# Performance work log

Hardware: AMD Instinct MI355X
Metric: run time of the kernel (lower is better)

## Reference

```python
import math
import jax, jax.numpy as jnp
import numpy as np

STRATEGY = 'small'
K_PEAKS = 2
BW = math.radians(15.0)
HIGH_RATIO = 0.3
LOW_RATIO = 0.2
ALPHA = 1.2
BETA = 0.8
N_BINS = 180


def setup_inputs() -> dict:
    key = jax.random.key(0)
    k1, k2, k3 = jax.random.split(key, 3)
    x = jax.random.normal(k1, (16, 256, 128, 128), dtype=jnp.float32)
    w_in = jax.random.normal(k2, (16, 256), dtype=jnp.float32) * 0.06    # proj_in 1x1 conv weight [c_mid, C]
    w_out = jax.random.normal(k3, (256, 16), dtype=jnp.float32) * 0.25   # proj_out 1x1 conv weight [C, c_mid]
    return {"x": x, "w_in": w_in, "w_out": w_out}


def _forward(x, w_in, w_out):
    B, C, H, W = x.shape
    pi = jnp.float32(math.pi)
    cy, cx = H // 2, W // 2
    y = jnp.arange(H, dtype=jnp.float32)[:, None]
    xg = jnp.arange(W, dtype=jnp.float32)[None, :]
    r = jnp.sqrt((y - cy) ** 2 + (xg - cx) ** 2)                 # [H, W]
    theta = jnp.arctan2(y - cy, xg - cx) + pi                    # [H, W] in [0, 2pi]
    r_max = float(min(cy, cx))

    # 1x1 conv in
    x_proj = jnp.einsum('mc,bchw->bmhw', w_in, x)                # [B, c_mid, H, W]

    fs = jnp.fft.fftshift(jnp.fft.fft2(x_proj, norm='ortho'), axes=(-2, -1))
    mag = jnp.abs(fs)                                            # [B, c_mid, H, W]

    # ---- peak direction detection (180-bin angular histogram of high-freq energy) ----
    theta_mod = theta % pi
    high_mask = (r > HIGH_RATIO * r_max).astype(jnp.float32)     # [H, W]
    bin_edges = jnp.linspace(0.0, math.pi, N_BINS + 1, dtype=jnp.float32)
    mag_avg = mag.mean(axis=1)                                   # [B, H, W]
    weighted = (mag_avg * high_mask).reshape(B, -1)              # [B, H*W]
    bin_idx = jnp.clip(jnp.searchsorted(bin_edges, theta_mod.reshape(-1), side='left') - 1, 0, N_BINS - 1)
    energy = jax.vmap(lambda w: jax.ops.segment_sum(w, bin_idx, num_segments=N_BINS))(weighted)  # [B, 180]

    # smooth with [0.25, 0.5, 0.25], zero padding
    ep = jnp.pad(energy, ((0, 0), (1, 1)))
    es = 0.25 * ep[:, :-2] + 0.5 * ep[:, 1:-1] + 0.25 * ep[:, 2:]  # [B, 180]

    mean_e = es.mean(axis=-1, keepdims=True)
    is_peak = (es > mean_e) & (es > jnp.roll(es, 1, axis=-1)) & (es > jnp.roll(es, -1, axis=-1))
    vals = jnp.where(is_peak, es, -jnp.inf)
    topv, topi = jax.lax.top_k(vals, K_PEAKS)                    # [B, k]
    count = jnp.sum(topv > -jnp.inf, axis=-1)                    # [B] number of valid peaks (<= k)
    amax = jnp.argmax(es, axis=-1)                               # fallback when no peak found
    topi = jnp.where((count > 0)[:, None], topi, amax[:, None])
    eff = jnp.maximum(count, 1)
    pos = jnp.minimum(jnp.arange(K_PEAKS)[None, :], (eff - 1)[:, None])  # pad with last valid peak
    final_idx = jnp.take_along_axis(topi, pos, axis=1)           # [B, k]
    bin_center = (bin_edges[:-1] + bin_edges[1:]) * 0.5
    peak_angles = bin_center[final_idx]                          # [B, k]

    # ---- gain map (channel-independent) ----
    if STRATEGY == 'small':
        pa = peak_angles
        base_mask = high_mask
    else:
        pa = (peak_angles + pi / 2) % pi
        base_mask = (r <= LOW_RATIO * r_max).astype(jnp.float32)
    diff = jnp.abs(theta[None, None] - pa[:, :, None, None])     # [B, k, H, W]
    diff = jnp.minimum(diff, pi - diff)
    in_region = (diff <= BW) & (base_mask[None, None] > 0)
    enh = jnp.any(in_region, axis=1).astype(jnp.float32)         # [B, H, W]
    gain = jnp.where(enh > 0, jnp.float32(ALPHA), jnp.float32(1.0))
    other_high = high_mask[None] * (1.0 - enh)
    gain = gain * (1.0 - other_high) + other_high * BETA         # [B, H, W]

    fs_enh = fs * gain[:, None, :, :]
    x_enh = jnp.fft.ifft2(jnp.fft.ifftshift(fs_enh, axes=(-2, -1)), norm='ortho').real
    out = jnp.einsum('cm,bmhw->bchw', w_out, x_enh)
    return x + out


def reference(x, w_in, w_out):
    return _forward(x, w_in, w_out)
```

## Files before the change

kernel.cpp:

```cpp
#include <hip/hip_runtime.h>
#include <math.h>

#define NPX 16384

static constexpr float  PI_F   = 3.14159265358979323846f;
static constexpr double PI_D   = 3.14159265358979323846;
static constexpr double STEP_D = PI_D / 180.0;
static constexpr double BW_D   = 15.0 * (PI_D / 180.0);

typedef float f4 __attribute__((ext_vector_type(4)));
typedef float f2 __attribute__((ext_vector_type(2)));

__device__ __forceinline__ int swz(int r, int c) {
    return (r << 7) | (c ^ (r ^ (r >> 1)));
}
__device__ __forceinline__ int brev7(int x) { return (int)(__brev((unsigned)x) >> 25); }
__device__ __forceinline__ float2 cadd(float2 a, float2 b){ return make_float2(a.x+b.x, a.y+b.y); }
__device__ __forceinline__ float2 csub(float2 a, float2 b){ return make_float2(a.x-b.x, a.y-b.y); }
__device__ __forceinline__ float2 cmul(float2 a, float re, float im){
    return make_float2(a.x*re - a.y*im, a.x*im + a.y*re);
}
__device__ __forceinline__ double edge_d(int i) {
    return (i >= 180) ? PI_D : (double)i * STEP_D;
}

__global__ void k0_tables(double* __restrict__ theta_d, int* __restrict__ bin_hi,
                          double* __restrict__ energy) {
    int p = blockIdx.x * blockDim.x + threadIdx.x;
    if (p < NPX) {
        int h = p >> 7, w = p & 127;
        double dy = (double)(h - 64), dx = (double)(w - 64);
        double theta = atan2(dy, dx) + PI_D;
        theta_d[p] = theta;
        double v = fmod(theta, PI_D);
        int cnt = 0;
        for (int i = 0; i <= 180; ++i) cnt += (edge_d(i) < v) ? 1 : 0;
        int bin = cnt - 1;
        if (bin < 0) bin = 0;
        if (bin > 179) bin = 179;
        int r2 = (h - 64)*(h - 64) + (w - 64)*(w - 64);
        bool high = (r2 >= 369);
        bin_hi[p] = high ? bin : -1;
    }
    if (blockIdx.x == 0) {
        for (int i = threadIdx.x; i < 16 * 180; i += blockDim.x) energy[i] = 0.0;
    }
}

__global__ __launch_bounds__(256, 1) void k1_proj(const float* __restrict__ x,
        const float* __restrict__ w_in, float* __restrict__ xproj) {
    int b  = blockIdx.y;
    int t4 = blockIdx.x * blockDim.x + threadIdx.x;
    const f4* xb = (const f4*)(x + (size_t)b * 256 * NPX);
    f4 acc[16];
    #pragma unroll
    for (int m = 0; m < 16; ++m) acc[m] = (f4)0.0f;
    #pragma unroll 8
    for (int c = 0; c < 256; ++c) {
        f4 xv = xb[(size_t)c * (NPX/4) + t4];
        #pragma unroll
        for (int m = 0; m < 16; ++m) {
            float wv = w_in[m * 256 + c];
            acc[m] += wv * xv;
        }
    }
    f4* xp = (f4*)(xproj + (size_t)b * 16 * NPX);
    #pragma unroll
    for (int m = 0; m < 16; ++m) xp[(size_t)m * (NPX/4) + t4] = acc[m];
}

__global__ __launch_bounds__(1024) void k_fft_fwd(const float* __restrict__ xproj,
        float2* __restrict__ fs, const int* __restrict__ bin_hi,
        double* __restrict__ energy) {
    extern __shared__ float2 lds[];
    __shared__ float twr[64], twi[64];
    __shared__ double histp[8][180];
    const int tid = threadIdx.x;
    const int img = blockIdx.x;
    if (tid < 64) {
        float ang = (float)tid * (PI_F / 64.0f);
        twr[tid] = cosf(ang);
        twi[tid] = sinf(ang);
    }
    if (tid < 180) {
        #pragma unroll
        for (int g = 0; g < 8; ++g) histp[g][tid] = 0.0;
    }
    const float* src = xproj + (size_t)img * NPX;
    #pragma unroll
    for (int it = 0; it < 16; ++it) {
        int p = tid + it * 1024;
        lds[swz(p >> 7, p & 127)] = make_float2(src[p], 0.0f);
    }
    __syncthreads();
    #pragma unroll
    for (int dim = 0; dim < 2; ++dim) {
        #pragma unroll
        for (int s = 0; s <= 4; s += 2) {
            const int q = 32 >> s;
            #pragma unroll
            for (int it = 0; it < 4; ++it) {
                int fb = tid + it * 1024;
                int o = fb & 127;
                int bfi = fb >> 7;
                int p = bfi & (q - 1);
                int g = bfi >> (5 - s);
                int P = g * (128 >> s) + p;
                int k1 = p << s;
                float tc = twr[k1],   ts = twi[k1];
                float uc = twr[2*k1], us = twi[2*k1];
                int e0, e1, e2, e3;
                if (dim == 0) { e0=swz(o,P); e1=swz(o,P+q); e2=swz(o,P+2*q); e3=swz(o,P+3*q); }
                else          { e0=swz(P,o); e1=swz(P+q,o); e2=swz(P+2*q,o); e3=swz(P+3*q,o); }
                float2 a = lds[e0], b = lds[e1], c = lds[e2], d = lds[e3];
                float2 u0 = cadd(a, c);
                float2 u1 = cmul(csub(a, c), tc, -ts);
                float2 v0 = cadd(b, d);
                float2 v1 = cmul(csub(b, d), -ts, -tc);
                lds[e0] = cadd(u0, v0);
                lds[e1] = cmul(csub(u0, v0), uc, -us);
                lds[e2] = cadd(u1, v1);
                lds[e3] = cmul(csub(u1, v1), uc, -us);
            }
            __syncthreads();
        }
        #pragma unroll
        for (int it = 0; it < 8; ++it) {
            int fb = tid + it * 1024;
            int o = fb & 127;
            int g = fb >> 7;
            int e0, e1;
            if (dim == 0) { e0 = swz(o, 2*g); e1 = swz(o, 2*g+1); }
            else          { e0 = swz(2*g, o); e1 = swz(2*g+1, o); }
            float2 a = lds[e0], b = lds[e1];
            lds[e0] = cadd(a, b);
            lds[e1] = csub(a, b);
        }
        __syncthreads();
    }
    float2* dst = fs + (size_t)img * NPX;
    const int bofs = (img >> 4) * 180;
    const int grp = tid >> 7;
    #pragma unroll
    for (int it = 0; it < 16; ++it) {
        int p = tid + it * 1024;
        int r = p >> 7, c = p & 127;
        float2 v = lds[swz(r, c)];
        dst[p] = v;
        int pix = ((brev7(r) ^ 64) << 7) | (brev7(c) ^ 64);
        int bh = bin_hi[pix];
        if (bh >= 0) {
            double m = sqrt((double)v.x * (double)v.x + (double)v.y * (double)v.y);
            atomicAdd(&histp[grp][bh], m);
        }
    }
    __syncthreads();
    if (tid < 180) {
        double s = 0.0;
        #pragma unroll
        for (int g = 0; g < 8; ++g) s += histp[g][tid];
        atomicAdd(&energy[bofs + tid], s);
    }
}

__global__ void k3_peaks(const double* __restrict__ energy, const double* __restrict__ theta_d,
                         const int* __restrict__ bin_hi, float* __restrict__ gain_s) {
    __shared__ double e[180], es[180];
    __shared__ double pa[2];
    int b = blockIdx.x, tid = threadIdx.x;
    if (tid < 180) e[tid] = energy[b * 180 + tid];
    __syncthreads();
    if (tid < 180) {
        double l = (tid > 0)   ? e[tid-1] : 0.0;
        double r = (tid < 179) ? e[tid+1] : 0.0;
        es[tid] = 0.25*l + 0.5*e[tid] + 0.25*r;
    }
    __syncthreads();
    if (tid == 0) {
        double sum = 0.0;
        for (int i = 0; i < 180; ++i) sum += es[i];
        double mean = sum / 180.0;
        double v0 = -INFINITY, v1 = -INFINITY;
        int   i0 = -1, i1 = -1;
        for (int i = 0; i < 180; ++i) {
            double prev = es[(i + 179) % 180];
            double nxt  = es[(i + 1) % 180];
            bool pk = (es[i] > mean) && (es[i] > prev) && (es[i] > nxt);
            if (pk) {
                double v = es[i];
                if (v > v0)      { v1 = v0; i1 = i0; v0 = v; i0 = i; }
                else if (v > v1) { v1 = v;  i1 = i; }
            }
        }
        int idx0, idx1;
        if (i0 < 0) {
            double mv = es[0]; int mi = 0;
            for (int i = 1; i < 180; ++i) if (es[i] > mv) { mv = es[i]; mi = i; }
            idx0 = idx1 = mi;
        } else if (i1 < 0) { idx0 = idx1 = i0; }
        else               { idx0 = i0; idx1 = i1; }
        pa[0] = (edge_d(idx0) + edge_d(idx0 + 1)) * 0.5;
        pa[1] = (edge_d(idx1) + edge_d(idx1 + 1)) * 0.5;
    }
    __syncthreads();
    double pa0 = pa[0], pa1 = pa[1];
    for (int p = tid; p < NPX; p += blockDim.x) {
        int r = p >> 7, c = p & 127;
        int pix = ((brev7(r) ^ 64) << 7) | (brev7(c) ^ 64);
        double th = theta_d[pix];
        bool high = bin_hi[pix] >= 0;
        double d0 = fabs(th - pa0); d0 = fmin(d0, PI_D - d0);
        double d1 = fabs(th - pa1); d1 = fmin(d1, PI_D - d1);
        bool enh = ((d0 <= BW_D) || (d1 <= BW_D)) && high;
        float g = enh ? 1.2f : (high ? 0.8f : 1.0f);
        gain_s[(size_t)b * NPX + p] = g * (1.0f / 16384.0f);
    }
}

__global__ __launch_bounds__(1024) void k_fft_inv(const float2* __restrict__ fs,
        const float* __restrict__ gain_s, float* __restrict__ xe) {
    extern __shared__ float2 lds[];
    __shared__ float twr[64], twi[64];
    const int tid = threadIdx.x;
    const int img = blockIdx.x;
    if (tid < 64) {
        float ang = (float)tid * (PI_F / 64.0f);
        twr[tid] = cosf(ang);
        twi[tid] = sinf(ang);
    }
    const float2* src = fs + (size_t)img * NPX;
    const float* gb = gain_s + (size_t)(img >> 4) * NPX;
    #pragma unroll
    for (int it = 0; it < 16; ++it) {
        int p = tid + it * 1024;
        float g = gb[p];
        float2 v = src[p];
        lds[swz(p >> 7, p & 127)] = make_float2(v.x * g, v.y * g);
    }
    __syncthreads();
    #pragma unroll
    for (int dim = 0; dim < 2; ++dim) {
        #pragma unroll
        for (int it = 0; it < 8; ++it) {
            int fb = tid + it * 1024;
            int o = fb & 127;
            int g = fb >> 7;
            int e0, e1;
            if (dim == 0) { e0 = swz(o, 2*g); e1 = swz(o, 2*g+1); }
            else          { e0 = swz(2*g, o); e1 = swz(2*g+1, o); }
            float2 a = lds[e0], b = lds[e1];
            lds[e0] = cadd(a, b);
            lds[e1] = csub(a, b);
        }
        __syncthreads();
        #pragma unroll
        for (int s = 4; s >= 0; s -= 2) {
            const int q = 32 >> s;
            #pragma unroll
            for (int it = 0; it < 4; ++it) {
                int fb = tid + it * 1024;
                int o = fb & 127;
                int bfi = fb >> 7;
                int p = bfi & (q - 1);
                int g = bfi >> (5 - s);
                int P = g * (128 >> s) + p;
                int k1 = p << s;
                float tc = twr[k1],   ts = twi[k1];
                float uc = twr[2*k1], us = twi[2*k1];
                int e0, e1, e2, e3;
                if (dim == 0) { e0=swz(o,P); e1=swz(o,P+q); e2=swz(o,P+2*q); e3=swz(o,P+3*q); }
                else          { e0=swz(P,o); e1=swz(P+q,o); e2=swz(P+2*q,o); e3=swz(P+3*q,o); }
                float2 o0 = lds[e0], o1 = lds[e1], o2 = lds[e2], o3 = lds[e3];
                float2 t1 = cmul(o1, uc, us);
                float2 u0 = cadd(o0, t1);
                float2 v0 = csub(o0, t1);
                float2 t3 = cmul(o3, uc, us);
                float2 u1 = cadd(o2, t3);
                float2 v1 = csub(o2, t3);
                float2 ta = cmul(u1, tc, ts);
                float2 tb = cmul(v1, -ts, tc);
                lds[e0] = cadd(u0, ta);
                lds[e2] = csub(u0, ta);
                lds[e1] = cadd(v0, tb);
                lds[e3] = csub(v0, tb);
            }
            __syncthreads();
        }
    }
    float* dstx = xe + (size_t)img * NPX;
    #pragma unroll
    for (int it = 0; it < 16; ++it) {
        int p = tid + it * 1024;
        dstx[p] = lds[swz(p >> 7, p & 127)].x;
    }
}

__global__ __launch_bounds__(256, 1) void k5_out(const float* __restrict__ x,
        const float* __restrict__ w_out, const float* __restrict__ xe,
        float* __restrict__ out) {
    int b = blockIdx.z, ct = blockIdx.y, pt = blockIdx.x, t = threadIdx.x;
    int p4 = pt * 256 + t;
    const f4* xeb = (const f4*)(xe + (size_t)b * 16 * NPX);
    f4 xv[16];
    #pragma unroll
    for (int m = 0; m < 16; ++m) xv[m] = xeb[(size_t)m * (NPX/4) + p4];
    #pragma unroll 8
    for (int cc = 0; cc < 16; ++cc) {
        int c = ct * 16 + cc;
        size_t base = ((size_t)b * 256 + c) * NPX;
        f4 a = ((const f4*)(x + base))[p4];
        #pragma unroll
        for (int m = 0; m < 16; ++m) {
            float wv = w_out[c * 16 + m];
            a += wv * xv[m];
        }
        __builtin_nontemporal_store(a, (f4*)(out + base) + p4);
    }
}

extern "C" void kernel_launch(void* const* d_in, const int* in_sizes, int n_in,
                              void* d_out, int out_size, void* d_ws, size_t ws_size,
                              hipStream_t stream) {
    const float* x     = (const float*)d_in[0];
    const float* w_in  = (const float*)d_in[1];
    const float* w_out = (const float*)d_in[2];
    float* out = (float*)d_out;
    char* ws = (char*)d_ws;

    double* theta_d = (double*)(ws);
    int*    bin_hi  = (int*)   (ws + 0x20000);
    double* energy  = (double*)(ws + 0x30000);
    float*  gain_s  = (float*) (ws + 0x40000);
    float*  xpe     = (float*) (ws + 0x140000);
    float2* fs = (float2*)((char*)d_out + (size_t)234881024);

    (void)hipFuncSetAttribute((const void*)k_fft_fwd,
            hipFuncAttributeMaxDynamicSharedMemorySize, 131072);
    (void)hipFuncSetAttribute((const void*)k_fft_inv,
            hipFuncAttributeMaxDynamicSharedMemorySize, 131072);

    k0_tables<<<dim3(64), dim3(256), 0, stream>>>(theta_d, bin_hi, energy);
    k1_proj  <<<dim3(16, 16), dim3(256), 0, stream>>>(x, w_in, xpe);
    k_fft_fwd<<<dim3(256), dim3(1024), 131072, stream>>>(xpe, fs, bin_hi, energy);
    k3_peaks <<<dim3(16), dim3(256), 0, stream>>>(energy, theta_d, bin_hi, gain_s);
    k_fft_inv<<<dim3(256), dim3(1024), 131072, stream>>>(fs, gain_s, xpe);
    k5_out   <<<dim3(16, 16, 16), dim3(256), 0, stream>>>(x, w_out, xpe, out);
}
```

Before: 273.1 us.

## Split projection channel reduction across two blocks and vectorize FFT input loads

The input projection kernel now splits the 256-channel reduction into two halves over a new grid dimension, doubling the block count from 256 to 512 so more of the GPU is busy during the bandwidth-heavy read of x. The two partial sums go to scratch space inside the output buffer and are added when the forward FFT loads its input, which is now read as float4. The inverse FFT load is also vectorized, reading spectrum and gain in wider chunks. The cost is an extra partial buffer to write and read back, and the scratch layout inside the output buffer is rearranged.

```diff
diff --git a/kernel.cpp b/kernel.cpp
--- a/kernel.cpp
+++ b/kernel.cpp
@@ -48,28 +48,28 @@
 }
 
 __global__ __launch_bounds__(256, 1) void k1_proj(const float* __restrict__ x,
-        const float* __restrict__ w_in, float* __restrict__ xproj) {
-    int b  = blockIdx.y;
+        const float* __restrict__ w_in, float* __restrict__ xpp) {
+    int b = blockIdx.y, z = blockIdx.z;
     int t4 = blockIdx.x * blockDim.x + threadIdx.x;
-    const f4* xb = (const f4*)(x + (size_t)b * 256 * NPX);
+    const f4* xb = (const f4*)(x + ((size_t)b * 256 + (size_t)z * 128) * NPX);
     f4 acc[16];
     #pragma unroll
     for (int m = 0; m < 16; ++m) acc[m] = (f4)0.0f;
-    #pragma unroll 8
-    for (int c = 0; c < 256; ++c) {
+    #pragma unroll 16
+    for (int c = 0; c < 128; ++c) {
         f4 xv = xb[(size_t)c * (NPX/4) + t4];
         #pragma unroll
         for (int m = 0; m < 16; ++m) {
-            float wv = w_in[m * 256 + c];
+            float wv = w_in[m * 256 + z * 128 + c];
             acc[m] += wv * xv;
         }
     }
-    f4* xp = (f4*)(xproj + (size_t)b * 16 * NPX);
+    f4* xp = (f4*)xpp + ((size_t)z * 256 + b * 16) * (NPX/4);
     #pragma unroll
     for (int m = 0; m < 16; ++m) xp[(size_t)m * (NPX/4) + t4] = acc[m];
 }
 
-__global__ __launch_bounds__(1024) void k_fft_fwd(const float* __restrict__ xproj,
+__global__ __launch_bounds__(1024) void k_fft_fwd(const float* __restrict__ xpp,
         float2* __restrict__ fs, const int* __restrict__ bin_hi,
         double* __restrict__ energy) {
     extern __shared__ float2 lds[];
@@ -86,11 +86,18 @@
         #pragma unroll
         for (int g = 0; g < 8; ++g) histp[g][tid] = 0.0;
     }
-    const float* src = xproj + (size_t)img * NPX;
-    #pragma unroll
-    for (int it = 0; it < 16; ++it) {
-        int p = tid + it * 1024;
-        lds[swz(p >> 7, p & 127)] = make_float2(src[p], 0.0f);
+    const f4* s0 = (const f4*)xpp + (size_t)img * (NPX/4);
+    const f4* s1 = (const f4*)xpp + (size_t)(256 + img) * (NPX/4);
+    #pragma unroll
+    for (int it = 0; it < 4; ++it) {
+        int p4 = tid + it * 1024;
+        f4 v = s0[p4] + s1[p4];
+        int pb = p4 * 4;
+        #pragma unroll
+        for (int j = 0; j < 4; ++j) {
+            int p = pb + j;
+            lds[swz(p >> 7, p & 127)] = make_float2(v[j], 0.0f);
+        }
     }
     __syncthreads();
     #pragma unroll
@@ -228,14 +235,16 @@
         twr[tid] = cosf(ang);
         twi[tid] = sinf(ang);
     }
-    const float2* src = fs + (size_t)img * NPX;
-    const float* gb = gain_s + (size_t)(img >> 4) * NPX;
-    #pragma unroll
-    for (int it = 0; it < 16; ++it) {
-        int p = tid + it * 1024;
-        float g = gb[p];
-        float2 v = src[p];
-        lds[swz(p >> 7, p & 127)] = make_float2(v.x * g, v.y * g);
+    const f4* srcv = (const f4*)(fs + (size_t)img * NPX);
+    const f2* gbv  = (const f2*)(gain_s + (size_t)(img >> 4) * NPX);
+    #pragma unroll
+    for (int it = 0; it < 8; ++it) {
+        int q = tid + it * 1024;
+        f4 v = srcv[q];
+        f2 g = gbv[q];
+        int p = q * 2;
+        lds[swz(p >> 7, p & 127)]             = make_float2(v.x * g.x, v.y * g.x);
+        lds[swz((p+1) >> 7, (p+1) & 127)]     = make_float2(v.z * g.y, v.w * g.y);
     }
     __syncthreads();
     #pragma unroll
@@ -331,8 +340,9 @@
     int*    bin_hi  = (int*)   (ws + 0x20000);
     double* energy  = (double*)(ws + 0x30000);
     float*  gain_s  = (float*) (ws + 0x40000);
-    float*  xpe     = (float*) (ws + 0x140000);
-    float2* fs = (float2*)((char*)d_out + (size_t)234881024);
+    float*  xe      = (float*) (ws + 0x140000);
+    float*  xpp = (float*)((char*)d_out + ((size_t)128 << 20));
+    float2* fs  = (float2*)((char*)d_out + ((size_t)224 << 20));
 
     (void)hipFuncSetAttribute((const void*)k_fft_fwd,
             hipFuncAttributeMaxDynamicSharedMemorySize, 131072);
@@ -340,9 +350,9 @@
             hipFuncAttributeMaxDynamicSharedMemorySize, 131072);
 
     k0_tables<<<dim3(64), dim3(256), 0, stream>>>(theta_d, bin_hi, energy);
-    k1_proj  <<<dim3(16, 16), dim3(256), 0, stream>>>(x, w_in, xpe);
-    k_fft_fwd<<<dim3(256), dim3(1024), 131072, stream>>>(xpe, fs, bin_hi, energy);
+    k1_proj  <<<dim3(16, 16, 2), dim3(256), 0, stream>>>(x, w_in, xpp);
+    k_fft_fwd<<<dim3(256), dim3(1024), 131072, stream>>>(xpp, fs, bin_hi, energy);
     k3_peaks <<<dim3(16), dim3(256), 0, stream>>>(energy, theta_d, bin_hi, gain_s);
-    k_fft_inv<<<dim3(256), dim3(1024), 131072, stream>>>(fs, gain_s, xpe);
-    k5_out   <<<dim3(16, 16, 16), dim3(256), 0, stream>>>(x, w_out, xpe, out);
-}
+    k_fft_inv<<<dim3(256), dim3(1024), 131072, stream>>>(fs, gain_s, xe);
+    k5_out   <<<dim3(16, 16, 16), dim3(256), 0, stream>>>(x, w_out, xe, out);
+}
```

Result: faster. 255.5 us (-6.4%).
